# Optimization experiments

Hardware: AMD Instinct MI355X
Metric: run time of the kernel (lower is better)

Reference implementation:

```python
import jax, jax.numpy as jnp
import numpy as np

D = 128   # hidden_dims
H = 8     # head_num
ALPHA = 0.5
EPS = 1e-5


def setup_inputs() -> dict:
    key = jax.random.key(0)
    ks = jax.random.split(key, 16)
    B, S = 2, 2048
    s = 0.02
    inp = {
        'x': jax.random.normal(ks[0], (B, S, D), jnp.float32),
        'adj_matrix': jax.random.randint(ks[1], (S, S), 0, 2, jnp.int32),
        'Wq': jax.random.normal(ks[2], (D, D * H), jnp.float32) * s,
        'bq': jnp.zeros((D * H,), jnp.float32),
        'Wk': jax.random.normal(ks[3], (D, D * H), jnp.float32) * s,
        'bk': jnp.zeros((D * H,), jnp.float32),
        'Wv': jax.random.normal(ks[4], (D, D * H), jnp.float32) * s,
        'bv': jnp.zeros((D * H,), jnp.float32),
        'Wo': jax.random.normal(ks[5], (D * H, D), jnp.float32) * s,
        'bo': jnp.zeros((D,), jnp.float32),
        'g1': jnp.ones((D,), jnp.float32), 'be1': jnp.zeros((D,), jnp.float32),
        'g2': jnp.ones((D,), jnp.float32), 'be2': jnp.zeros((D,), jnp.float32),
        'W1': jax.random.normal(ks[6], (D, D), jnp.float32) * s,
        'b1': jnp.zeros((D,), jnp.float32),
        'W2': jax.random.normal(ks[7], (D, D), jnp.float32) * s,
        'b2': jnp.zeros((D,), jnp.float32),
    }
    return inp


def _layernorm(x, g, b):
    mu = jnp.mean(x, axis=-1, keepdims=True)
    var = jnp.var(x, axis=-1, keepdims=True)
    return (x - mu) * jax.lax.rsqrt(var + EPS) * g + b


def reference(x, adj_matrix, Wq, bq, Wk, bk, Wv, bv, Wo, bo, g1, be1, g2, be2, W1, b1, W2, b2):
    B, S, _ = x.shape
    q = (x @ Wq + bq).reshape(B, S, H, D)
    k = (x @ Wk + bk).reshape(B, S, H, D)
    v = (x @ Wv + bv).reshape(B, S, H, D)
    scores = jnp.einsum('bqhd,bkhd->bhqk', q, k) / jnp.sqrt(jnp.float32(D))
    soft_mask = ALPHA * adj_matrix.astype(jnp.float32) + (1.0 - ALPHA)  # [S,S]
    scores = scores * soft_mask  # broadcast over B,H
    attn = jax.nn.softmax(scores, axis=-1)
    out = jnp.einsum('bhqk,bkhd->bqhd', attn, v).reshape(B, S, H * D)
    out = out @ Wo + bo
    h = _layernorm(x + out, g1, be1)
    ff = jax.nn.relu(h @ W1 + b1) @ W2 + b2
    y = _layernorm(h + ff, g2, be2)
    return y, attn
```

## Files before the change

kernel.cpp:

```cpp
#include <hip/hip_runtime.h>
#include <hip/hip_bf16.h>

#define HD 128
#define NH 8
#define SQ 2048
#define NROWS 4096
#define RSQRT_D 0.08838834764831845f

typedef __bf16 bf16;
typedef bf16 bf16x8 __attribute__((ext_vector_type(8)));
typedef float f32x4 __attribute__((ext_vector_type(4)));

__device__ __forceinline__ f32x4 mfma16(bf16x8 a, bf16x8 b, f32x4 c) {
  return __builtin_amdgcn_mfma_f32_16x16x32_bf16(a, b, c, 0, 0, 0);
}
__device__ __forceinline__ bf16x8 ld8(const bf16* p) { return *(const bf16x8*)p; }
__device__ __forceinline__ unsigned short bfu(float v) {
  return __builtin_bit_cast(unsigned short, (bf16)v);
}
__device__ __forceinline__ unsigned packbf2(float a, float b) {
  return (unsigned)bfu(a) | ((unsigned)bfu(b) << 16);
}
__device__ __forceinline__ void gload_lds16(const void* g, void* l) {
  __builtin_amdgcn_global_load_lds(
      (const __attribute__((address_space(1))) void*)g,
      (__attribute__((address_space(3))) void*)l, 16, 0, 0);
}

__global__ void k_prep_a(const float* __restrict__ x, const int* __restrict__ adj,
                         bf16* __restrict__ xb, unsigned char* __restrict__ mask8) {
  int idx = blockIdx.x * 256 + threadIdx.x;
  if (idx < NROWS * HD) { xb[idx] = (bf16)x[idx]; return; }
  int j = idx - NROWS * HD;
  if (j < (SQ * SQ / 4)) {
    int4 a = ((const int4*)adj)[j];
    uchar4 m;
    m.x = (unsigned char)a.x; m.y = (unsigned char)a.y;
    m.z = (unsigned char)a.z; m.w = (unsigned char)a.w;
    ((uchar4*)mask8)[j] = m;
  }
}

__global__ void k_prep_w(const float* __restrict__ Wq, const float* __restrict__ Wk,
                         const float* __restrict__ Wv, const float* __restrict__ Wo,
                         const float* __restrict__ W1, const float* __restrict__ W2,
                         bf16* __restrict__ WqkvT, bf16* __restrict__ WoT,
                         bf16* __restrict__ W1T, bf16* __restrict__ W2T) {
  int idx = blockIdx.x * 256 + threadIdx.x;
  if (idx < 3072 * 128) {
    int n = idx >> 7, kk = idx & 127;
    int sel = n >> 10, nn = n & 1023;
    const float* W = (sel == 0) ? Wq : (sel == 1 ? Wk : Wv);
    WqkvT[idx] = (bf16)W[kk * 1024 + nn];
    return;
  }
  int j = idx - 3072 * 128;
  if (j < 128 * 1024) { int n = j >> 10, kk = j & 1023; WoT[j] = (bf16)Wo[kk * 128 + n]; return; }
  j -= 128 * 1024;
  if (j < 16384) { int n = j >> 7, kk = j & 127; W1T[j] = (bf16)W1[kk * 128 + n]; return; }
  j -= 16384;
  if (j < 16384) { int n = j >> 7, kk = j & 127; W2T[j] = (bf16)W2[kk * 128 + n]; return; }
}

__global__ __launch_bounds__(256, 4) void k_qkv(
    const bf16* __restrict__ xb, const bf16* __restrict__ WqkvT,
    const float* __restrict__ bq, const float* __restrict__ bk, const float* __restrict__ bv,
    bf16* __restrict__ qT, bf16* __restrict__ kT, bf16* __restrict__ vT) {
  const int bid = blockIdx.x;
  const int m0 = (bid & 63) << 6;
  const int n0 = (bid >> 6) << 6;
  const int tid = threadIdx.x;
  const int w = tid >> 6, lane = tid & 63, lo = lane & 15, hi = lane >> 4;
  const int mw = m0 + ((w >> 1) << 5);
  const int nw = n0 + ((w & 1) << 5);
  bf16x8 av[2][4], bw[2][4];
#pragma unroll
  for (int ms = 0; ms < 2; ++ms)
#pragma unroll
    for (int ks = 0; ks < 4; ++ks)
      av[ms][ks] = ld8(xb + (size_t)(mw + ms * 16 + lo) * 128 + ks * 32 + hi * 8);
#pragma unroll
  for (int ns = 0; ns < 2; ++ns)
#pragma unroll
    for (int ks = 0; ks < 4; ++ks)
      bw[ns][ks] = ld8(WqkvT + (size_t)(nw + ns * 16 + lo) * 128 + ks * 32 + hi * 8);
  const f32x4 z4 = {0.f, 0.f, 0.f, 0.f};
  f32x4 acc[2][2] = {{z4, z4}, {z4, z4}};
#pragma unroll
  for (int ms = 0; ms < 2; ++ms)
#pragma unroll
    for (int ns = 0; ns < 2; ++ns)
#pragma unroll
      for (int ks = 0; ks < 4; ++ks)
        acc[ms][ns] = mfma16(av[ms][ks], bw[ns][ks], acc[ms][ns]);
#pragma unroll
  for (int ns = 0; ns < 2; ++ns) {
    const int n = nw + ns * 16 + lo;
    const int sel = n >> 10, nn = n & 1023;
    const float bia = (sel == 0 ? bq : sel == 1 ? bk : bv)[nn];
    const int hh = nn >> 7, d = nn & 127;
#pragma unroll
    for (int ms = 0; ms < 2; ++ms) {
      const int mb = mw + ms * 16 + hi * 4;
      const int bb = mb >> 11, s = mb & 2047;
      if (sel == 0) {
#pragma unroll
        for (int r = 0; r < 4; ++r)
          qT[(size_t)((bb * 8 + hh) * 2048 + s + r) * 128 + d] =
              (bf16)((acc[ms][ns][r] + bia) * RSQRT_D);
      } else if (sel == 1) {
#pragma unroll
        for (int r = 0; r < 4; ++r)
          kT[(size_t)((bb * 8 + hh) * 2048 + s + r) * 128 + d] = (bf16)(acc[ms][ns][r] + bia);
      } else {
        ushort4 pk;
        pk.x = bfu(acc[ms][ns][0] + bia);
        pk.y = bfu(acc[ms][ns][1] + bia);
        pk.z = bfu(acc[ms][ns][2] + bia);
        pk.w = bfu(acc[ms][ns][3] + bia);
        *(ushort4*)(vT + (size_t)((bb * 8 + hh) * 128 + d) * 2048 + s) = pk;
      }
    }
  }
}

__global__ __launch_bounds__(512, 2) void k_attn(
    const bf16* __restrict__ qT, const bf16* __restrict__ kT,
    const bf16* __restrict__ vT, const unsigned char* __restrict__ mask8,
    float* __restrict__ attn_out, bf16* __restrict__ Oc) {
  __shared__ __align__(16) char kbuf[2][8192];
  __shared__ __align__(16) char vbuf[2][8192];
  __shared__ __align__(16) char stash[8][1024];
  __shared__ float red2[128];

  const int lbid = blockIdx.x;
  const int work = ((lbid & 7) << 5) + (lbid >> 3);
  const int bh = work >> 4;
  const int q0 = (work & 15) << 7;
  const int b = bh >> 3, h = bh & 7;
  const int tid = threadIdx.x;
  const int w = tid >> 6, lane = tid & 63, lo = lane & 15, hi = lane >> 4;

  const bf16* Qh = qT + (size_t)bh * SQ * HD;
  const bf16* Kh = kT + (size_t)bh * SQ * HD;
  const bf16* Vh = vT + (size_t)bh * HD * SQ;
  const int qg = q0 + w * 16 + lo;

  const int krow = (w << 2) + (lane >> 4);
  const int kslog = (lane & 15) ^ (krow & 7);
  const bf16* kg = Kh + (size_t)krow * HD + kslog * 8;
  const int vrow = (w << 4) + (lane >> 2);
  const bf16* vg = Vh + (size_t)vrow * SQ + (lane & 3) * 8;

  bf16x8 qf[4];
#pragma unroll
  for (int ks = 0; ks < 4; ++ks)
    qf[ks] = ld8(Qh + (size_t)qg * HD + ks * 32 + hi * 8);

  const f32x4 z4 = {0.f, 0.f, 0.f, 0.f};
  f32x4 acc[8];
#pragma unroll
  for (int ds = 0; ds < 8; ++ds) acc[ds] = z4;
  float ssum = 0.f;

  gload_lds16(kg, &kbuf[0][w * 1024]);
  gload_lds16(vg, &vbuf[0][w * 1024]);
  __syncthreads();

  for (int i = 0; i < 64; ++i) {
    const int kvA = i << 5;
    const int cur = i & 1;
    if (i < 63) {
      gload_lds16(kg + (size_t)(kvA + 32) * HD, &kbuf[cur ^ 1][w * 1024]);
      gload_lds16(vg + (kvA + 32), &vbuf[cur ^ 1][w * 1024]);
    }
    const char* kb = kbuf[cur];
    const char* vb = vbuf[cur];
#pragma unroll
    for (int t = 0; t < 2; ++t) {
      const int row = t * 16 + lo;
      bf16x8 af[4];
#pragma unroll
      for (int ks = 0; ks < 4; ++ks)
        af[ks] = *(const bf16x8*)(kb + row * 256 + ((((ks << 2) + hi)) ^ (row & 7)) * 16);
      f32x4 c = z4;
#pragma unroll
      for (int ks = 0; ks < 4; ++ks) c = mfma16(af[ks], qf[ks], c);
      const unsigned mu = *(const unsigned*)(mask8 + (size_t)qg * SQ + kvA + t * 16 + hi * 4);
      float p0 = __expf(c[0] * (0.5f + 0.5f * (float)(mu & 0xff)));
      float p1 = __expf(c[1] * (0.5f + 0.5f * (float)((mu >> 8) & 0xff)));
      float p2 = __expf(c[2] * (0.5f + 0.5f * (float)((mu >> 16) & 0xff)));
      float p3 = __expf(c[3] * (0.5f + 0.5f * (float)((mu >> 24) & 0xff)));
      ssum += (p0 + p1) + (p2 + p3);
      *(uint2*)(stash[w] + lo * 64 + ((t * 32 + hi * 8) ^ ((lo & 3) << 4))) =
          make_uint2(packbf2(p0, p1), packbf2(p2, p3));
    }
    bf16x8 pa = *(const bf16x8*)(stash[w] + lo * 64 + ((hi * 16) ^ ((lo & 3) << 4)));
#pragma unroll
    for (int ds = 0; ds < 8; ++ds) {
      bf16x8 vf = *(const bf16x8*)(vb + (ds * 16 + lo) * 64 + hi * 16);
      acc[ds] = mfma16(pa, vf, acc[ds]);
    }
    __syncthreads();
  }

  ssum += __shfl_xor(ssum, 16);
  ssum += __shfl_xor(ssum, 32);
  if (hi == 0) red2[w * 16 + lo] = 1.0f / ssum;
  __syncthreads();

#pragma unroll
  for (int ds = 0; ds < 8; ++ds)
#pragma unroll
    for (int r = 0; r < 4; ++r) {
      const int qrow = w * 16 + hi * 4 + r;
      Oc[(size_t)(b * SQ + q0 + qrow) * (NH * HD) + h * HD + ds * 16 + lo] =
          (bf16)(acc[ds][r] * red2[qrow]);
    }

  const float rinv = red2[w * 16 + lo];
  float* abase = attn_out + (size_t)bh * SQ * SQ + (size_t)qg * SQ;
  gload_lds16(kg, &kbuf[0][w * 1024]);
  __syncthreads();
  for (int i = 0; i < 64; ++i) {
    const int kvA = i << 5;
    const int cur = i & 1;
    if (i < 63)
      gload_lds16(kg + (size_t)(kvA + 32) * HD, &kbuf[cur ^ 1][w * 1024]);
    const char* kb = kbuf[cur];
#pragma unroll
    for (int t = 0; t < 2; ++t) {
      const int row = t * 16 + lo;
      bf16x8 af[4];
#pragma unroll
      for (int ks = 0; ks < 4; ++ks)
        af[ks] = *(const bf16x8*)(kb + row * 256 + ((((ks << 2) + hi)) ^ (row & 7)) * 16);
      f32x4 c = z4;
#pragma unroll
      for (int ks = 0; ks < 4; ++ks) c = mfma16(af[ks], qf[ks], c);
      const unsigned mu = *(const unsigned*)(mask8 + (size_t)qg * SQ + kvA + t * 16 + hi * 4);
      f32x4 o;
      o[0] = __expf(c[0] * (0.5f + 0.5f * (float)(mu & 0xff))) * rinv;
      o[1] = __expf(c[1] * (0.5f + 0.5f * (float)((mu >> 8) & 0xff))) * rinv;
      o[2] = __expf(c[2] * (0.5f + 0.5f * (float)((mu >> 16) & 0xff))) * rinv;
      o[3] = __expf(c[3] * (0.5f + 0.5f * (float)((mu >> 24) & 0xff))) * rinv;
      __builtin_nontemporal_store(o, (f32x4*)(abase + kvA + t * 16 + hi * 4));
    }
    __syncthreads();
  }
}

__global__ __launch_bounds__(256, 4) void k_owo(
    const bf16* __restrict__ Oc, const bf16* __restrict__ WoT,
    const float* __restrict__ bo, const float* __restrict__ x,
    const float* __restrict__ g1, const float* __restrict__ be1,
    float* __restrict__ hf, bf16* __restrict__ hb) {
  __shared__ __align__(16) float hbuf[16 * 128];
  const int m0 = blockIdx.x * 16;
  const int tid = threadIdx.x;
  const int w = tid >> 6, lane = tid & 63, lo = lane & 15, hi = lane >> 4;
  const int nw = w * 32;
  const f32x4 z4 = {0.f, 0.f, 0.f, 0.f};
  f32x4 acc[2] = {z4, z4};
#pragma unroll 4
  for (int kk = 0; kk < 32; ++kk) {
    bf16x8 a = ld8(Oc + (size_t)(m0 + lo) * 1024 + kk * 32 + hi * 8);
#pragma unroll
    for (int ns = 0; ns < 2; ++ns) {
      bf16x8 bb = ld8(WoT + (size_t)(nw + ns * 16 + lo) * 1024 + kk * 32 + hi * 8);
      acc[ns] = mfma16(a, bb, acc[ns]);
    }
  }
#pragma unroll
  for (int ns = 0; ns < 2; ++ns) {
    const int n = nw + ns * 16 + lo;
    const float bia = bo[n];
#pragma unroll
    for (int r = 0; r < 4; ++r) {
      const int mr = hi * 4 + r;
      hbuf[mr * 128 + n] = acc[ns][r] + bia + x[(size_t)(m0 + mr) * 128 + n];
    }
  }
  __syncthreads();
  const float2 g = *(const float2*)(g1 + lane * 2);
  const float2 be = *(const float2*)(be1 + lane * 2);
#pragma unroll
  for (int rr = 0; rr < 4; ++rr) {
    const int row = w * 4 + rr;
    float2 v = *(float2*)&hbuf[row * 128 + lane * 2];
    float s = v.x + v.y, sq = v.x * v.x + v.y * v.y;
#pragma unroll
    for (int off = 32; off; off >>= 1) { s += __shfl_xor(s, off); sq += __shfl_xor(sq, off); }
    const float mean = s * (1.f / 128.f);
    const float var = sq * (1.f / 128.f) - mean * mean;
    const float rstd = rsqrtf(var + 1e-5f);
    const float y0 = (v.x - mean) * rstd * g.x + be.x;
    const float y1 = (v.y - mean) * rstd * g.y + be.y;
    const size_t o = (size_t)(m0 + row) * 128 + lane * 2;
    *(float2*)(hf + o) = make_float2(y0, y1);
    *(unsigned*)(hb + o) = packbf2(y0, y1);
  }
}

__global__ __launch_bounds__(256, 4) void k_ffn(
    const bf16* __restrict__ hb, const float* __restrict__ hf,
    const bf16* __restrict__ W1T, const bf16* __restrict__ W2T,
    const float* __restrict__ b1, const float* __restrict__ b2,
    const float* __restrict__ g2, const float* __restrict__ be2,
    float* __restrict__ yout) {
  __shared__ __align__(16) bf16 s1[16 * 136];
  __shared__ __align__(16) float ybuf[16 * 128];
  const int m0 = blockIdx.x * 16;
  const int tid = threadIdx.x;
  const int w = tid >> 6, lane = tid & 63, lo = lane & 15, hi = lane >> 4;
  const int nw = w * 32;
  const f32x4 z4 = {0.f, 0.f, 0.f, 0.f};
  f32x4 a1[2] = {z4, z4};
#pragma unroll
  for (int kk = 0; kk < 4; ++kk) {
    bf16x8 a = ld8(hb + (size_t)(m0 + lo) * 128 + kk * 32 + hi * 8);
#pragma unroll
    for (int ns = 0; ns < 2; ++ns)
      a1[ns] = mfma16(a, ld8(W1T + (size_t)(nw + ns * 16 + lo) * 128 + kk * 32 + hi * 8), a1[ns]);
  }
#pragma unroll
  for (int ns = 0; ns < 2; ++ns) {
    const int n = nw + ns * 16 + lo;
    const float bia = b1[n];
#pragma unroll
    for (int r = 0; r < 4; ++r)
      s1[(hi * 4 + r) * 136 + n] = (bf16)fmaxf(a1[ns][r] + bia, 0.f);
  }
  __syncthreads();
  f32x4 a2[2] = {z4, z4};
#pragma unroll
  for (int kk = 0; kk < 4; ++kk) {
    bf16x8 a = *(const bf16x8*)&s1[lo * 136 + kk * 32 + hi * 8];
#pragma unroll
    for (int ns = 0; ns < 2; ++ns)
      a2[ns] = mfma16(a, ld8(W2T + (size_t)(nw + ns * 16 + lo) * 128 + kk * 32 + hi * 8), a2[ns]);
  }
#pragma unroll
  for (int ns = 0; ns < 2; ++ns) {
    const int n = nw + ns * 16 + lo;
    const float bia = b2[n];
#pragma unroll
    for (int r = 0; r < 4; ++r) {
      const int mr = hi * 4 + r;
      ybuf[mr * 128 + n] = a2[ns][r] + bia + hf[(size_t)(m0 + mr) * 128 + n];
    }
  }
  __syncthreads();
  const float2 g = *(const float2*)(g2 + lane * 2);
  const float2 be = *(const float2*)(be2 + lane * 2);
#pragma unroll
  for (int rr = 0; rr < 4; ++rr) {
    const int row = w * 4 + rr;
    float2 v = *(float2*)&ybuf[row * 128 + lane * 2];
    float s = v.x + v.y, sq = v.x * v.x + v.y * v.y;
#pragma unroll
    for (int off = 32; off; off >>= 1) { s += __shfl_xor(s, off); sq += __shfl_xor(sq, off); }
    const float mean = s * (1.f / 128.f);
    const float var = sq * (1.f / 128.f) - mean * mean;
    const float rstd = rsqrtf(var + 1e-5f);
    const float y0 = (v.x - mean) * rstd * g.x + be.x;
    const float y1 = (v.y - mean) * rstd * g.y + be.y;
    *(float2*)(yout + (size_t)(m0 + row) * 128 + lane * 2) = make_float2(y0, y1);
  }
}

extern "C" void kernel_launch(void* const* d_in, const int* in_sizes, int n_in,
                              void* d_out, int out_size, void* d_ws, size_t ws_size,
                              hipStream_t stream) {
  const float* x  = (const float*)d_in[0];
  const int* adj  = (const int*)d_in[1];
  const float* Wq = (const float*)d_in[2];  const float* bq = (const float*)d_in[3];
  const float* Wk = (const float*)d_in[4];  const float* bk = (const float*)d_in[5];
  const float* Wv = (const float*)d_in[6];  const float* bv = (const float*)d_in[7];
  const float* Wo = (const float*)d_in[8];  const float* bo = (const float*)d_in[9];
  const float* g1 = (const float*)d_in[10]; const float* be1 = (const float*)d_in[11];
  const float* g2 = (const float*)d_in[12]; const float* be2 = (const float*)d_in[13];
  const float* W1 = (const float*)d_in[14]; const float* b1 = (const float*)d_in[15];
  const float* W2 = (const float*)d_in[16]; const float* b2 = (const float*)d_in[17];

  char* ws = (char*)d_ws;
  bf16* xb     = (bf16*)(ws + 0);
  bf16* WqkvT  = (bf16*)(ws + 1048576);
  bf16* WoT    = (bf16*)(ws + 1835008);
  bf16* W1T    = (bf16*)(ws + 2097152);
  bf16* W2T    = (bf16*)(ws + 2129920);
  unsigned char* mask8 = (unsigned char*)(ws + 2162688);
  bf16* qT     = (bf16*)(ws + 6356992);
  bf16* kT     = (bf16*)(ws + 14745600);
  bf16* vT     = (bf16*)(ws + 23134208);
  bf16* Oc     = (bf16*)(ws + 31522816);
  float* hf    = (float*)(ws + 39911424);
  bf16* hb     = (bf16*)(ws + 42008576);

  float* yout = (float*)d_out;
  float* attn_out = yout + (size_t)NROWS * HD;

  k_prep_a<<<6144, 256, 0, stream>>>(x, adj, xb, mask8);
  k_prep_w<<<2176, 256, 0, stream>>>(Wq, Wk, Wv, Wo, W1, W2, WqkvT, WoT, W1T, W2T);
  k_qkv<<<3072, 256, 0, stream>>>(xb, WqkvT, bq, bk, bv, qT, kT, vT);
  k_attn<<<256, 512, 0, stream>>>(qT, kT, vT, mask8, attn_out, Oc);
  k_owo<<<256, 256, 0, stream>>>(Oc, WoT, bo, x, g1, be1, hf, hb);
  k_ffn<<<256, 256, 0, stream>>>(hb, hf, W1T, W2T, b1, b2, g2, be2, yout);
}
```

Before: 226.0 us.

## Split attention into 64-query blocks of 4 waves and fold log2e into exp2

The attention kernel now runs 512 blocks of 256 threads, each covering 64 query rows instead of 128. Each thread issues two K and two V async loads per stage so the 32-row KV tiles still fill. The softmax exponent folds the 0.5 mask scaling and log2(e) into one fma feeding exp2f. The aim is better CU occupancy and load balance on MI355X plus cheaper exp math, at the cost of twice the total K/V global traffic because each block streams the full KV sequence.

Measured after the change: 209.8 us (median of 2 runs). 7.1% less time.

```diff
diff --git a/kernel.cpp b/kernel.cpp
--- a/kernel.cpp
+++ b/kernel.cpp
@@ -6,6 +6,7 @@
 #define SQ 2048
 #define NROWS 4096
 #define RSQRT_D 0.08838834764831845f
+#define L2EH 0.72134752044f
 
 typedef __bf16 bf16;
 typedef bf16 bf16x8 __attribute__((ext_vector_type(8)));
@@ -124,19 +125,19 @@
   }
 }
 
-__global__ __launch_bounds__(512, 2) void k_attn(
+__global__ __launch_bounds__(256, 2) void k_attn(
     const bf16* __restrict__ qT, const bf16* __restrict__ kT,
     const bf16* __restrict__ vT, const unsigned char* __restrict__ mask8,
     float* __restrict__ attn_out, bf16* __restrict__ Oc) {
   __shared__ __align__(16) char kbuf[2][8192];
   __shared__ __align__(16) char vbuf[2][8192];
-  __shared__ __align__(16) char stash[8][1024];
-  __shared__ float red2[128];
+  __shared__ __align__(16) char stash[4][1024];
+  __shared__ float red2[64];
 
   const int lbid = blockIdx.x;
-  const int work = ((lbid & 7) << 5) + (lbid >> 3);
-  const int bh = work >> 4;
-  const int q0 = (work & 15) << 7;
+  const int work = ((lbid & 7) << 6) + (lbid >> 3);
+  const int bh = work >> 5;
+  const int q0 = (work & 31) << 6;
   const int b = bh >> 3, h = bh & 7;
   const int tid = threadIdx.x;
   const int w = tid >> 6, lane = tid & 63, lo = lane & 15, hi = lane >> 4;
@@ -146,11 +147,14 @@
   const bf16* Vh = vT + (size_t)bh * HD * SQ;
   const int qg = q0 + w * 16 + lo;
 
-  const int krow = (w << 2) + (lane >> 4);
-  const int kslog = (lane & 15) ^ (krow & 7);
-  const bf16* kg = Kh + (size_t)krow * HD + kslog * 8;
-  const int vrow = (w << 4) + (lane >> 2);
-  const bf16* vg = Vh + (size_t)vrow * SQ + (lane & 3) * 8;
+  const int krow0 = (w << 2) + (lane >> 4);
+  const int krow1 = 16 + krow0;
+  const bf16* kg0 = Kh + (size_t)krow0 * HD + (((lane & 15) ^ (krow0 & 7)) << 3);
+  const bf16* kg1 = Kh + (size_t)krow1 * HD + (((lane & 15) ^ (krow1 & 7)) << 3);
+  const int vrow0 = (w << 4) + (lane >> 2);
+  const int vrow1 = 64 + vrow0;
+  const bf16* vg0 = Vh + (size_t)vrow0 * SQ + ((lane & 3) << 3);
+  const bf16* vg1 = Vh + (size_t)vrow1 * SQ + ((lane & 3) << 3);
 
   bf16x8 qf[4];
 #pragma unroll
@@ -163,16 +167,21 @@
   for (int ds = 0; ds < 8; ++ds) acc[ds] = z4;
   float ssum = 0.f;
 
-  gload_lds16(kg, &kbuf[0][w * 1024]);
-  gload_lds16(vg, &vbuf[0][w * 1024]);
+  gload_lds16(kg0, &kbuf[0][w * 1024]);
+  gload_lds16(kg1, &kbuf[0][4096 + w * 1024]);
+  gload_lds16(vg0, &vbuf[0][w * 1024]);
+  gload_lds16(vg1, &vbuf[0][4096 + w * 1024]);
   __syncthreads();
 
   for (int i = 0; i < 64; ++i) {
     const int kvA = i << 5;
     const int cur = i & 1;
     if (i < 63) {
-      gload_lds16(kg + (size_t)(kvA + 32) * HD, &kbuf[cur ^ 1][w * 1024]);
-      gload_lds16(vg + (kvA + 32), &vbuf[cur ^ 1][w * 1024]);
+      const size_t ko = (size_t)(kvA + 32) * HD;
+      gload_lds16(kg0 + ko, &kbuf[cur ^ 1][w * 1024]);
+      gload_lds16(kg1 + ko, &kbuf[cur ^ 1][4096 + w * 1024]);
+      gload_lds16(vg0 + (kvA + 32), &vbuf[cur ^ 1][w * 1024]);
+      gload_lds16(vg1 + (kvA + 32), &vbuf[cur ^ 1][4096 + w * 1024]);
     }
     const char* kb = kbuf[cur];
     const char* vb = vbuf[cur];
@@ -187,10 +196,10 @@
 #pragma unroll
       for (int ks = 0; ks < 4; ++ks) c = mfma16(af[ks], qf[ks], c);
       const unsigned mu = *(const unsigned*)(mask8 + (size_t)qg * SQ + kvA + t * 16 + hi * 4);
-      float p0 = __expf(c[0] * (0.5f + 0.5f * (float)(mu & 0xff)));
-      float p1 = __expf(c[1] * (0.5f + 0.5f * (float)((mu >> 8) & 0xff)));
-      float p2 = __expf(c[2] * (0.5f + 0.5f * (float)((mu >> 16) & 0xff)));
-      float p3 = __expf(c[3] * (0.5f + 0.5f * (float)((mu >> 24) & 0xff)));
+      float p0 = exp2f(c[0] * fmaf((float)(mu & 0xff),         L2EH, L2EH));
+      float p1 = exp2f(c[1] * fmaf((float)((mu >> 8) & 0xff),  L2EH, L2EH));
+      float p2 = exp2f(c[2] * fmaf((float)((mu >> 16) & 0xff), L2EH, L2EH));
+      float p3 = exp2f(c[3] * fmaf((float)((mu >> 24) & 0xff), L2EH, L2EH));
       ssum += (p0 + p1) + (p2 + p3);
       *(uint2*)(stash[w] + lo * 64 + ((t * 32 + hi * 8) ^ ((lo & 3) << 4))) =
           make_uint2(packbf2(p0, p1), packbf2(p2, p3));
@@ -220,13 +229,17 @@
 
   const float rinv = red2[w * 16 + lo];
   float* abase = attn_out + (size_t)bh * SQ * SQ + (size_t)qg * SQ;
-  gload_lds16(kg, &kbuf[0][w * 1024]);
+  gload_lds16(kg0, &kbuf[0][w * 1024]);
+  gload_lds16(kg1, &kbuf[0][4096 + w * 1024]);
   __syncthreads();
   for (int i = 0; i < 64; ++i) {
     const int kvA = i << 5;
     const int cur = i & 1;
-    if (i < 63)
-      gload_lds16(kg + (size_t)(kvA + 32) * HD, &kbuf[cur ^ 1][w * 1024]);
+    if (i < 63) {
+      const size_t ko = (size_t)(kvA + 32) * HD;
+      gload_lds16(kg0 + ko, &kbuf[cur ^ 1][w * 1024]);
+      gload_lds16(kg1 + ko, &kbuf[cur ^ 1][4096 + w * 1024]);
+    }
     const char* kb = kbuf[cur];
 #pragma unroll
     for (int t = 0; t < 2; ++t) {
@@ -240,10 +253,10 @@
       for (int ks = 0; ks < 4; ++ks) c = mfma16(af[ks], qf[ks], c);
       const unsigned mu = *(const unsigned*)(mask8 + (size_t)qg * SQ + kvA + t * 16 + hi * 4);
       f32x4 o;
-      o[0] = __expf(c[0] * (0.5f + 0.5f * (float)(mu & 0xff))) * rinv;
-      o[1] = __expf(c[1] * (0.5f + 0.5f * (float)((mu >> 8) & 0xff))) * rinv;
-      o[2] = __expf(c[2] * (0.5f + 0.5f * (float)((mu >> 16) & 0xff))) * rinv;
-      o[3] = __expf(c[3] * (0.5f + 0.5f * (float)((mu >> 24) & 0xff))) * rinv;
+      o[0] = exp2f(c[0] * fmaf((float)(mu & 0xff),         L2EH, L2EH)) * rinv;
+      o[1] = exp2f(c[1] * fmaf((float)((mu >> 8) & 0xff),  L2EH, L2EH)) * rinv;
+      o[2] = exp2f(c[2] * fmaf((float)((mu >> 16) & 0xff), L2EH, L2EH)) * rinv;
+      o[3] = exp2f(c[3] * fmaf((float)((mu >> 24) & 0xff), L2EH, L2EH)) * rinv;
       __builtin_nontemporal_store(o, (f32x4*)(abase + kvA + t * 16 + hi * 4));
     }
     __syncthreads();
@@ -403,7 +416,7 @@
   k_prep_a<<<6144, 256, 0, stream>>>(x, adj, xb, mask8);
   k_prep_w<<<2176, 256, 0, stream>>>(Wq, Wk, Wv, Wo, W1, W2, WqkvT, WoT, W1T, W2T);
   k_qkv<<<3072, 256, 0, stream>>>(xb, WqkvT, bq, bk, bv, qT, kT, vT);
-  k_attn<<<256, 512, 0, stream>>>(qT, kT, vT, mask8, attn_out, Oc);
+  k_attn<<<512, 256, 0, stream>>>(qT, kT, vT, mask8, attn_out, Oc);
   k_owo<<<256, 256, 0, stream>>>(Oc, WoT, bo, x, g1, be1, hf, hb);
   k_ffn<<<256, 256, 0, stream>>>(hb, hf, W1T, W2T, b1, b2, g2, be2, yout);
 }
```
